# Kernel tuning notes

Measured on AMD Instinct MI355X. Metric: run time of the kernel, lower is better.

## Reference

```python
import jax, jax.numpy as jnp
import numpy as np

N = 50000      # nodes
E = 800000     # edges
CIN = 128
CH = 128
COUT = 64
EPS = 1e-5     # BatchNorm eps


def setup_inputs() -> dict:
    key = jax.random.key(0)
    ks = jax.random.split(key, 16)
    s = 0.1  # weight scale for numerical stability
    return {
        "x": jax.random.normal(ks[0], (N, CIN), jnp.float32),
        "edge_index": jax.random.randint(ks[1], (2, E), 0, N, jnp.int32),
        "edge_weights": jax.random.uniform(ks[2], (E,), jnp.float32),
        "w1": jax.random.normal(ks[3], (CIN, CH), jnp.float32) * s,
        "b1": jnp.zeros((CH,), jnp.float32),
        "bn1_g": jnp.ones((CH,), jnp.float32),
        "bn1_b": jnp.zeros((CH,), jnp.float32),
        "bn1_m": jax.random.normal(ks[4], (CH,), jnp.float32) * 0.1,
        "bn1_v": jax.random.uniform(ks[5], (CH,), jnp.float32) + 0.5,
        "conv_ws": jax.random.normal(ks[6], (2, CH, CH), jnp.float32) * s,
        "conv_bs": jnp.zeros((2, CH), jnp.float32),
        "bns_g": jnp.ones((2, CH), jnp.float32),
        "bns_b": jnp.zeros((2, CH), jnp.float32),
        "bns_m": jax.random.normal(ks[7], (2, CH), jnp.float32) * 0.1,
        "bns_v": jax.random.uniform(ks[8], (2, CH), jnp.float32) + 0.5,
        "lin1_w": jax.random.normal(ks[9], (CH, CH), jnp.float32) * s,
        "lin1_b": jnp.zeros((CH,), jnp.float32),
        "lin2_w": jax.random.normal(ks[10], (CH, COUT), jnp.float32) * s,
        "lin2_b": jnp.zeros((COUT,), jnp.float32),
    }


def _bn(h, g, b, m, v):
    # BatchNorm1d in eval mode: running statistics
    return (h - m) * jax.lax.rsqrt(v + EPS) * g + b


def _gcn(h, w, b, src, dst, norm, n):
    # GCNConv: out[dst] += norm_e * (h @ W)[src]  (self loops already in src/dst)
    h = h @ w
    msg = h[src] * norm[:, None]                 # [E+N, CH]
    return jax.ops.segment_sum(msg, dst, num_segments=n) + b


def reference(x, edge_index, edge_weights, w1, b1, bn1_g, bn1_b, bn1_m, bn1_v,
              conv_ws, conv_bs, bns_g, bns_b, bns_m, bns_v,
              lin1_w, lin1_b, lin2_w, lin2_b):
    n = x.shape[0]
    loop = jnp.arange(n, dtype=edge_index.dtype)
    src = jnp.concatenate([edge_index[0], loop])
    dst = jnp.concatenate([edge_index[1], loop])
    ew = jnp.concatenate([edge_weights, jnp.ones((n,), edge_weights.dtype)])
    # symmetric degree normalization (PyG gcn_norm)
    deg = jax.ops.segment_sum(ew, dst, num_segments=n)
    dis = jnp.where(deg > 0, jax.lax.rsqrt(deg), 0.0)
    norm = dis[src] * ew * dis[dst]

    lrelu = jax.nn.leaky_relu  # slope 0.01, matches F.leaky_relu default
    h = lrelu(_bn(_gcn(x, w1, b1, src, dst, norm, n), bn1_g, bn1_b, bn1_m, bn1_v))
    for i in range(conv_ws.shape[0]):
        h = lrelu(_bn(_gcn(h, conv_ws[i], conv_bs[i], src, dst, norm, n),
                      bns_g[i], bns_b[i], bns_m[i], bns_v[i]) + h)
    h = lrelu(h @ lin1_w + lin1_b)
    # dropout is identity in eval mode
    return h @ lin2_w + lin2_b
```

## Files before the change

### kernel.cpp

```cpp
#include <hip/hip_runtime.h>
#include <hip/hip_bf16.h>


constexpr int   NN    = 50000;
constexpr int   EE    = 800000;
constexpr int   CH    = 128;
constexpr int   SLOTS = 64;
constexpr int   NBUK  = 782;
constexpr int   RCAP  = 2048;
constexpr int   EPB   = 2048;
constexpr float EPS   = 1e-5f;

typedef __attribute__((ext_vector_type(8))) short bf16x8;
typedef __attribute__((ext_vector_type(4))) float f32x4;
typedef unsigned long long u64;
typedef unsigned short u16;

__device__ inline u16 f2bf_rne(float f) {
  unsigned u = __float_as_uint(f);
  unsigned r = u + 0x7fffu + ((u >> 16) & 1u);
  return (u16)(r >> 16);
}
__device__ inline float bf2f(unsigned h16) {
  return __uint_as_float(h16 << 16);
}


__global__ __launch_bounds__(256) void bin_kernel(const int* __restrict__ ei,
                                                  const float* __restrict__ ew,
                                                  unsigned* __restrict__ gcur,
                                                  u64* __restrict__ bins) {
  __shared__ unsigned cnt[NBUK];
  __shared__ unsigned base[NBUK];
  const int tid = threadIdx.x;
  for (int b = tid; b < NBUK; b += 256) cnt[b] = 0;
  __syncthreads();
  const int e0 = blockIdx.x * EPB;
  unsigned pk[8]; u16 bkt[8]; u16 rnk[8]; unsigned char dl[8];
  #pragma unroll
  for (int i = 0; i < 8; i++) {
    int e = e0 + i * 256 + tid;
    if (e < EE) {
      int s = ei[e], d = ei[EE + e];
      float w = ew[e];
      bkt[i] = (u16)(d >> 6);
      dl[i]  = (unsigned char)(d & 63);
      pk[i]  = ((unsigned)f2bf_rne(w) << 16) | (unsigned)s;
      rnk[i] = (u16)atomicAdd(&cnt[bkt[i]], 1u);
    } else bkt[i] = 0xffffu;
  }
  __syncthreads();
  for (int b = tid; b < NBUK; b += 256) {
    unsigned c = cnt[b];
    base[b] = c ? atomicAdd(&gcur[b * 16], c) : 0u;
  }
  __syncthreads();
  #pragma unroll
  for (int i = 0; i < 8; i++) {
    if (bkt[i] == 0xffffu) continue;
    unsigned pos = base[bkt[i]] + rnk[i];
    if (pos < RCAP)
      bins[(size_t)bkt[i] * RCAP + pos] = ((u64)dl[i] << 32) | pk[i];
  }
}


__global__ __launch_bounds__(256) void scatter_kernel(const unsigned* __restrict__ gcur,
                                                      const u64* __restrict__ bins,
                                                      unsigned* __restrict__ ell,
                                                      float* __restrict__ dis) {
  __shared__ unsigned rank[64];
  __shared__ float    wsum[64];
  const int b   = blockIdx.x;
  const int tid = threadIdx.x;
  if (tid < 64) { rank[tid] = 1u; wsum[tid] = 0.f; }
  __syncthreads();
  unsigned cnt = gcur[b * 16];
  if (cnt > RCAP) cnt = RCAP;
  const u64* src = bins + (size_t)b * RCAP;
  for (unsigned i = tid; i < cnt; i += 256) {
    u64 v = src[i];
    unsigned pk = (unsigned)v;
    unsigned dl = (unsigned)(v >> 32);
    unsigned r = atomicAdd(&rank[dl], 1u);
    if (r < SLOTS)
      ell[((size_t)(b * 64 + dl)) * SLOTS + r] = pk;
    atomicAdd(&wsum[dl], bf2f(pk >> 16));
  }
  __syncthreads();
  if (tid < 64) {
    int node = b * 64 + tid;
    if (node < NN) {
      unsigned c = rank[tid];
      if (c > SLOTS) c = SLOTS;
      ell[(size_t)node * SLOTS] = c;
      dis[node] = rsqrtf(1.0f + wsum[tid]);
    }
  }
}

constexpr int NB_WZ = (73728 + 384 + 255) / 256;

__global__ void wswz_kernel(
    const float* __restrict__ w1, const float* __restrict__ bn1_g, const float* __restrict__ bn1_v,
    const float* __restrict__ conv_ws, const float* __restrict__ bns_g, const float* __restrict__ bns_v,
    const float* __restrict__ lin1_w, const float* __restrict__ lin2_w,
    const float* __restrict__ b1, const float* __restrict__ bn1_b, const float* __restrict__ bn1_m,
    const float* __restrict__ conv_bs, const float* __restrict__ bns_b, const float* __restrict__ bns_m,
    u16* __restrict__ w1h, u16* __restrict__ w1l,
    u16* __restrict__ c0h, u16* __restrict__ c0l,
    u16* __restrict__ c1h, u16* __restrict__ c1l,
    u16* __restrict__ l1h, u16* __restrict__ l1l,
    u16* __restrict__ l2h, u16* __restrict__ l2l,
    float* __restrict__ beff)
{
  int idx = blockIdx.x * 256 + threadIdx.x;
  if (idx >= 73728) {
    int r = idx - 73728;
    if (r >= 384) return;
    int l = r >> 7, c = r & 127;
    float bc, gg, bb, mm, vv;
    if (l == 0) { bc = b1[c]; gg = bn1_g[c]; bb = bn1_b[c]; mm = bn1_m[c]; vv = bn1_v[c]; }
    else {
      int o = (l - 1) * 128 + c;
      bc = conv_bs[o]; gg = bns_g[o]; bb = bns_b[o]; mm = bns_m[o]; vv = bns_v[o];
    }
    beff[r] = (bc - mm) * gg * rsqrtf(vv + EPS) + bb;
    return;
  }
  const float* W; const float* g = nullptr; const float* v = nullptr;
  u16 *hi, *lo; int CO = 128; int local;
  if      (idx < 16384) { W = w1;              g = bn1_g;     v = bn1_v;     hi = w1h; lo = w1l; local = idx; }
  else if (idx < 32768) { W = conv_ws;         g = bns_g;     v = bns_v;     hi = c0h; lo = c0l; local = idx - 16384; }
  else if (idx < 49152) { W = conv_ws + 16384; g = bns_g+128; v = bns_v+128; hi = c1h; lo = c1l; local = idx - 32768; }
  else if (idx < 65536) { W = lin1_w;                                        hi = l1h; lo = l1l; local = idx - 49152; }
  else                  { W = lin2_w;                                        hi = l2h; lo = l2l; local = idx - 65536; CO = 64; }
  int k = local / CO, n = local % CO;
  float w = W[local];
  if (g) w *= g[n] * rsqrtf(v[n] + EPS);
  int NCT = CO / 16;
  int kchunk = k >> 5, kin = k & 31, quad = kin >> 3, j = kin & 7;
  int ct = n >> 4, l = (quad << 4) | (n & 15);
  size_t pos = ((size_t)(kchunk * NCT + ct) * 64 + l) * 8 + j;
  u16 h = f2bf_rne(w);
  hi[pos] = h;
  lo[pos] = f2bf_rne(w - bf2f(h));
}

__global__ __launch_bounds__(256) void gemm1_kernel(
    const float* __restrict__ Ain,
    const u16* __restrict__ Whi, const u16* __restrict__ Wlo,
    const float* __restrict__ dis, u16* __restrict__ Cout)
{
  __shared__ float lds[64][CH + 4];
  const int tid  = threadIdx.x;
  const int wave = tid >> 6;
  const int lane = tid & 63;
  const int quad = lane >> 4;
  const int mrow = lane & 15;
  const int row0 = blockIdx.x * 64;

  int arow = row0 + wave * 16 + mrow;
  if (arow >= NN) arow = NN - 1;

  bf16x8 ahi[4], alo[4];
  const float* Ar = Ain + (size_t)arow * CH;
  #pragma unroll
  for (int c = 0; c < 4; c++) {
    int off = c * 32 + quad * 8;
    float4 f0 = *(const float4*)(Ar + off);
    float4 f1 = *(const float4*)(Ar + off + 4);
    float f[8] = {f0.x, f0.y, f0.z, f0.w, f1.x, f1.y, f1.z, f1.w};
    #pragma unroll
    for (int j = 0; j < 8; j++) {
      u16 h = f2bf_rne(f[j]);
      ahi[c][j] = (short)h;
      alo[c][j] = (short)f2bf_rne(f[j] - bf2f(h));
    }
  }

  f32x4 acc[8];
  #pragma unroll
  for (int t = 0; t < 8; t++) acc[t] = (f32x4){0.f, 0.f, 0.f, 0.f};
  #pragma unroll
  for (int c = 0; c < 4; c++) {
    #pragma unroll
    for (int t = 0; t < 8; t++) {
      size_t base = ((size_t)(c * 8 + t) * 64 + lane) * 8;
      bf16x8 bh = *(const bf16x8*)(Whi + base);
      bf16x8 bl = *(const bf16x8*)(Wlo + base);
      acc[t] = __builtin_amdgcn_mfma_f32_16x16x32_bf16(ahi[c], bh, acc[t], 0, 0, 0);
      acc[t] = __builtin_amdgcn_mfma_f32_16x16x32_bf16(alo[c], bh, acc[t], 0, 0, 0);
      acc[t] = __builtin_amdgcn_mfma_f32_16x16x32_bf16(ahi[c], bl, acc[t], 0, 0, 0);
    }
  }

  #pragma unroll
  for (int t = 0; t < 8; t++)
    #pragma unroll
    for (int r = 0; r < 4; r++)
      lds[wave * 16 + quad * 4 + r][t * 16 + mrow] = acc[t][r];
  __syncthreads();

  #pragma unroll
  for (int i = tid; i < 64 * CH / 4; i += 256) {
    int row = (i * 4) / CH;
    int col = (i * 4) % CH;
    int grow = row0 + row;
    if (grow >= NN) continue;
    float rs = dis[grow];
    const float* lp = &lds[row][col];
    u16* cp = (u16*)Cout + (size_t)grow * CH + col;
    unsigned p0 = ((unsigned)f2bf_rne(lp[1] * rs) << 16) | f2bf_rne(lp[0] * rs);
    unsigned p1 = ((unsigned)f2bf_rne(lp[3] * rs) << 16) | f2bf_rne(lp[2] * rs);
    *(uint2*)cp = make_uint2(p0, p1);
  }
}

template<bool RES, bool WH>
__device__ __forceinline__ void gather4_grp(
    const u16* __restrict__ hwin, const unsigned* __restrict__ ell,
    const float* __restrict__ dis, const float* __restrict__ beff,
    const u16* __restrict__ res, u16* __restrict__ hout,
    unsigned* __restrict__ hsbase,
    int nbase, int lane, int sub, int grp)
{
  const int node = nbase + grp;
  const size_t ebase = (size_t)node * SLOTS + sub;
  unsigned w0 = ell[ebase];
  unsigned w1 = ell[ebase + 16];
  unsigned w2 = ell[ebase + 32];
  unsigned w3 = ell[ebase + 48];

  int cme = __shfl((int)w0, grp << 4); if (cme > SLOTS) cme = SLOTS;
  int c0 = __shfl((int)w0, 0),  c1 = __shfl((int)w0, 16);
  int c2 = __shfl((int)w0, 32), c3 = __shfl((int)w0, 48);
  int cmax = max(max(c0, c1), max(c2, c3)); if (cmax > SLOTS) cmax = SLOTS;

  float a[8] = {0.f, 0.f, 0.f, 0.f, 0.f, 0.f, 0.f, 0.f};
  const u16* hrow = hwin + sub * 8;

  for (int j = 0; j < cmax; j += 8) {
    uint4 hQ[8]; float wQ[8];
    #pragma unroll
    for (int u = 0; u < 8; u++) {
      int jj = j + u;
      int k = jj >> 4;
      unsigned wsel = k == 0 ? w0 : (k == 1 ? w1 : (k == 2 ? w2 : w3));
      unsigned e = (unsigned)__shfl((int)wsel, (grp << 4) | (jj & 15));
      float wv = (jj == 0) ? 1.0f : bf2f(e >> 16);
      unsigned s = (jj == 0) ? (unsigned)node : (e & 0xffffu);
      if (jj >= cme) { wv = 0.f; s = (unsigned)node; }
      wQ[u] = wv;
      hQ[u] = *(const uint4*)(hrow + (size_t)s * CH);
    }
    #pragma unroll
    for (int u = 0; u < 8; u++) {
      float w = wQ[u];
      a[0] = fmaf(w, bf2f(hQ[u].x & 0xffffu), a[0]); a[1] = fmaf(w, bf2f(hQ[u].x >> 16), a[1]);
      a[2] = fmaf(w, bf2f(hQ[u].y & 0xffffu), a[2]); a[3] = fmaf(w, bf2f(hQ[u].y >> 16), a[3]);
      a[4] = fmaf(w, bf2f(hQ[u].z & 0xffffu), a[4]); a[5] = fmaf(w, bf2f(hQ[u].z >> 16), a[5]);
      a[6] = fmaf(w, bf2f(hQ[u].w & 0xffffu), a[6]); a[7] = fmaf(w, bf2f(hQ[u].w >> 16), a[7]);
    }
  }

  float disd = dis[node];
  int c = sub * 8;
  float4 be0 = *(const float4*)(beff + c);
  float4 be1 = *(const float4*)(beff + c + 4);
  float y[8];
  y[0] = a[0] * disd + be0.x; y[1] = a[1] * disd + be0.y;
  y[2] = a[2] * disd + be0.z; y[3] = a[3] * disd + be0.w;
  y[4] = a[4] * disd + be1.x; y[5] = a[5] * disd + be1.y;
  y[6] = a[6] * disd + be1.z; y[7] = a[7] * disd + be1.w;
  if constexpr (RES) {
    uint4 rr = *(const uint4*)(res + (size_t)node * CH + c);
    y[0] += bf2f(rr.x & 0xffffu); y[1] += bf2f(rr.x >> 16);
    y[2] += bf2f(rr.y & 0xffffu); y[3] += bf2f(rr.y >> 16);
    y[4] += bf2f(rr.z & 0xffffu); y[5] += bf2f(rr.z >> 16);
    y[6] += bf2f(rr.w & 0xffffu); y[7] += bf2f(rr.w >> 16);
  }
  #pragma unroll
  for (int k = 0; k < 8; k++) y[k] = y[k] > 0.f ? y[k] : 0.01f * y[k];
  uint4 o;
  o.x = ((unsigned)f2bf_rne(y[1]) << 16) | f2bf_rne(y[0]);
  o.y = ((unsigned)f2bf_rne(y[3]) << 16) | f2bf_rne(y[2]);
  o.z = ((unsigned)f2bf_rne(y[5]) << 16) | f2bf_rne(y[4]);
  o.w = ((unsigned)f2bf_rne(y[7]) << 16) | f2bf_rne(y[6]);
  if constexpr (WH)
    *(uint4*)(hout + (size_t)node * CH + c) = o;
  *(uint4*)&hsbase[grp * 68 + sub * 4] = o;
}

template<bool RES>
__global__ __launch_bounds__(256, 6) void fuse_kernel(
    const u16* __restrict__ hwin,
    const unsigned* __restrict__ ell, const float* __restrict__ dis,
    const float* __restrict__ beff, const u16* __restrict__ res,
    const u16* __restrict__ Whi, const u16* __restrict__ Wlo,
    u16* __restrict__ hout, u16* __restrict__ hwout)
{
  __shared__ unsigned hs[16][68];
  const int tid  = threadIdx.x;
  const int wave = tid >> 6;
  const int lane = tid & 63;
  const int sub  = lane & 15;
  const int grp  = lane >> 4;
  const int row0 = blockIdx.x * 16;

  gather4_grp<RES, true>(hwin, ell, dis, beff, res, hout,
                         &hs[wave * 4][0], row0 + wave * 4, lane, sub, grp);
  __syncthreads();

  bf16x8 af[4];
  #pragma unroll
  for (int c = 0; c < 4; c++)
    af[c] = *(const bf16x8*)&hs[sub][c * 16 + grp * 4];

  f32x4 acc[2];
  #pragma unroll
  for (int t = 0; t < 2; t++) acc[t] = (f32x4){0.f, 0.f, 0.f, 0.f};
  #pragma unroll
  for (int c = 0; c < 4; c++) {
    #pragma unroll
    for (int t = 0; t < 2; t++) {
      size_t base = ((size_t)(c * 8 + wave * 2 + t) * 64 + lane) * 8;
      bf16x8 bh = *(const bf16x8*)(Whi + base);
      bf16x8 bl = *(const bf16x8*)(Wlo + base);
      acc[t] = __builtin_amdgcn_mfma_f32_16x16x32_bf16(af[c], bh, acc[t], 0, 0, 0);
      acc[t] = __builtin_amdgcn_mfma_f32_16x16x32_bf16(af[c], bl, acc[t], 0, 0, 0);
    }
  }

  #pragma unroll
  for (int r = 0; r < 4; r++) {
    int grow = row0 + grp * 4 + r;
    if (grow >= NN) continue;
    float rs = dis[grow];
    #pragma unroll
    for (int t = 0; t < 2; t++)
      hwout[(size_t)grow * CH + wave * 32 + t * 16 + sub] = f2bf_rne(acc[t][r] * rs);
  }
}

__global__ __launch_bounds__(256, 6) void fuse_last_kernel(
    const u16* __restrict__ hwin,
    const unsigned* __restrict__ ell, const float* __restrict__ dis,
    const float* __restrict__ beff, const u16* __restrict__ res,
    const u16* __restrict__ l1h, const u16* __restrict__ l1l,
    const float* __restrict__ b1,
    const u16* __restrict__ l2h, const u16* __restrict__ l2l,
    const float* __restrict__ b2, float* __restrict__ out)
{
  __shared__ unsigned hs[16][68];
  __shared__ float    fs[16][132];
  const int tid  = threadIdx.x;
  const int wave = tid >> 6;
  const int lane = tid & 63;
  const int sub  = lane & 15;
  const int grp  = lane >> 4;
  const int row0 = blockIdx.x * 16;

  gather4_grp<true, false>(hwin, ell, dis, beff, res, nullptr,
                           &hs[wave * 4][0], row0 + wave * 4, lane, sub, grp);
  __syncthreads();

  bf16x8 af[4];
  #pragma unroll
  for (int c = 0; c < 4; c++)
    af[c] = *(const bf16x8*)&hs[sub][c * 16 + grp * 4];

  f32x4 acc[2];
  #pragma unroll
  for (int t = 0; t < 2; t++) acc[t] = (f32x4){0.f, 0.f, 0.f, 0.f};
  #pragma unroll
  for (int c = 0; c < 4; c++) {
    #pragma unroll
    for (int t = 0; t < 2; t++) {
      size_t base = ((size_t)(c * 8 + wave * 2 + t) * 64 + lane) * 8;
      bf16x8 bh = *(const bf16x8*)(l1h + base);
      bf16x8 bl = *(const bf16x8*)(l1l + base);
      acc[t] = __builtin_amdgcn_mfma_f32_16x16x32_bf16(af[c], bh, acc[t], 0, 0, 0);
      acc[t] = __builtin_amdgcn_mfma_f32_16x16x32_bf16(af[c], bl, acc[t], 0, 0, 0);
    }
  }
  #pragma unroll
  for (int t = 0; t < 2; t++) {
    int col = wave * 32 + t * 16 + sub;
    float bb = b1[col];
    #pragma unroll
    for (int r = 0; r < 4; r++) {
      float x = acc[t][r] + bb;
      x = x > 0.f ? x : 0.01f * x;
      fs[grp * 4 + r][col] = x;
    }
  }
  __syncthreads();

  f32x4 acc2 = (f32x4){0.f, 0.f, 0.f, 0.f};
  #pragma unroll
  for (int c = 0; c < 4; c++) {
    bf16x8 ahi, alo;
    const float* lp = &fs[sub][c * 32 + grp * 8];
    float4 f0 = *(const float4*)lp;
    float4 f1 = *(const float4*)(lp + 4);
    float f[8] = {f0.x, f0.y, f0.z, f0.w, f1.x, f1.y, f1.z, f1.w};
    #pragma unroll
    for (int j = 0; j < 8; j++) {
      u16 h = f2bf_rne(f[j]);
      ahi[j] = (short)h;
      alo[j] = (short)f2bf_rne(f[j] - bf2f(h));
    }
    size_t base = ((size_t)(c * 4 + wave) * 64 + lane) * 8;
    bf16x8 bh = *(const bf16x8*)(l2h + base);
    bf16x8 bl = *(const bf16x8*)(l2l + base);
    acc2 = __builtin_amdgcn_mfma_f32_16x16x32_bf16(ahi, bh, acc2, 0, 0, 0);
    acc2 = __builtin_amdgcn_mfma_f32_16x16x32_bf16(alo, bh, acc2, 0, 0, 0);
    acc2 = __builtin_amdgcn_mfma_f32_16x16x32_bf16(ahi, bl, acc2, 0, 0, 0);
  }
  {
    float bb = b2[wave * 16 + sub];
    #pragma unroll
    for (int r = 0; r < 4; r++) {
      int grow = row0 + grp * 4 + r;
      if (grow < NN)
        out[(size_t)grow * 64 + wave * 16 + sub] = acc2[r] + bb;
    }
  }
}


extern "C" void kernel_launch(void* const* d_in, const int* in_sizes, int n_in,
                              void* d_out, int out_size, void* d_ws, size_t ws_size,
                              hipStream_t stream) {
  const float* x       = (const float*)d_in[0];
  const int*   ei      = (const int*)  d_in[1];
  const float* ew      = (const float*)d_in[2];
  const float* w1      = (const float*)d_in[3];
  const float* b1      = (const float*)d_in[4];
  const float* bn1_g   = (const float*)d_in[5];
  const float* bn1_b   = (const float*)d_in[6];
  const float* bn1_m   = (const float*)d_in[7];
  const float* bn1_v   = (const float*)d_in[8];
  const float* conv_ws = (const float*)d_in[9];
  const float* conv_bs = (const float*)d_in[10];
  const float* bns_g   = (const float*)d_in[11];
  const float* bns_b   = (const float*)d_in[12];
  const float* bns_m   = (const float*)d_in[13];
  const float* bns_v   = (const float*)d_in[14];
  const float* lin1_w  = (const float*)d_in[15];
  const float* lin1_b  = (const float*)d_in[16];
  const float* lin2_w  = (const float*)d_in[17];
  const float* lin2_b  = (const float*)d_in[18];
  float* out = (float*)d_out;

  size_t off = 0;
  auto alloc = [&](size_t elems) -> void* {
    void* p = (char*)d_ws + off * 4;
    off += (elems + 3) & ~(size_t)3;
    return p;
  };
  unsigned* gcur = (unsigned*)alloc(NBUK * 16);
  u64*      bins = (u64*)     alloc((size_t)NBUK * RCAP * 2);
  unsigned* ell  = (unsigned*)alloc((size_t)NN * SLOTS);
  float*    dis  = (float*)   alloc(NN);
  float*    beff = (float*)   alloc(3 * CH);
  u16*      hwa  = (u16*)     alloc((size_t)NN * CH / 2);
  u16*      hwb  = (u16*)     alloc((size_t)NN * CH / 2);
  u16*      h1   = (u16*)     alloc((size_t)NN * CH / 2);
  u16*      h2   = (u16*)     alloc((size_t)NN * CH / 2);
  u16* w1h = (u16*)alloc(CH * CH / 2); u16* w1l = (u16*)alloc(CH * CH / 2);
  u16* c0h = (u16*)alloc(CH * CH / 2); u16* c0l = (u16*)alloc(CH * CH / 2);
  u16* c1h = (u16*)alloc(CH * CH / 2); u16* c1l = (u16*)alloc(CH * CH / 2);
  u16* l1h = (u16*)alloc(CH * CH / 2); u16* l1l = (u16*)alloc(CH * CH / 2);
  u16* l2h = (u16*)alloc(CH * 64 / 2); u16* l2l = (u16*)alloc(CH * 64 / 2);

  const int nb_bin  = (EE + EPB - 1) / EPB;
  const int nb_gemm = (NN + 63) / 64;
  const int nb_fuse = (NN + 15) / 16;
  dim3 B(256);

  hipMemsetAsync(gcur, 0, NBUK * 16 * sizeof(unsigned), stream);
  bin_kernel    <<<nb_bin, B, 0, stream>>>(ei, ew, gcur, bins);
  scatter_kernel<<<NBUK,   B, 0, stream>>>(gcur, bins, ell, dis);

  wswz_kernel<<<NB_WZ, B, 0, stream>>>(w1, bn1_g, bn1_v, conv_ws, bns_g, bns_v,
      lin1_w, lin2_w, b1, bn1_b, bn1_m, conv_bs, bns_b, bns_m,
      w1h, w1l, c0h, c0l, c1h, c1l, l1h, l1l, l2h, l2l, beff);

  gemm1_kernel<<<nb_gemm, B, 0, stream>>>(x, w1h, w1l, dis, hwa);

  fuse_kernel<false><<<nb_fuse, B, 0, stream>>>(hwa, ell, dis, beff, nullptr,
      c0h, c0l, h1, hwb);

  fuse_kernel<true><<<nb_fuse, B, 0, stream>>>(hwb, ell, dis, beff + CH, h1,
      c1h, c1l, h2, hwa);

  fuse_last_kernel<<<nb_fuse, B, 0, stream>>>(hwa, ell, dis, beff + 2 * CH, h2,
      l1h, l1l, lin1_b, l2h, l2l, lin2_b, out);
}
```

Before: 333.7 us.

## Fuse binning with weight swizzle and scatter with first GEMM; stage fuse stores

Merges the edge-binning kernel and the weight-swizzle kernel into one launch by giving each a separate block range. It also fuses the ELL scatter and degree computation with the first GEMM, since both use 64-node blocks, so dis is taken from shared memory instead of global. In fuse_kernel, outputs are staged through LDS and written as coalesced 16-byte stores, which adds extra barriers. Together this removes two launches and reduces uncoalesced 2-byte global writes.

```diff
diff --git a/kernel.cpp b/kernel.cpp
--- a/kernel.cpp
+++ b/kernel.cpp
@@ -9,6 +9,8 @@
 constexpr int   NBUK  = 782;
 constexpr int   RCAP  = 2048;
 constexpr int   EPB   = 2048;
+constexpr int   NB_BIN = (EE + EPB - 1) / EPB;
+constexpr int   NB_WZ  = (73728 + 384 + 255) / 256;
 constexpr float EPS   = 1e-5f;
 
 typedef __attribute__((ext_vector_type(8))) short bf16x8;
@@ -26,82 +28,9 @@
 }
 
 
-__global__ __launch_bounds__(256) void bin_kernel(const int* __restrict__ ei,
-                                                  const float* __restrict__ ew,
-                                                  unsigned* __restrict__ gcur,
-                                                  u64* __restrict__ bins) {
-  __shared__ unsigned cnt[NBUK];
-  __shared__ unsigned base[NBUK];
-  const int tid = threadIdx.x;
-  for (int b = tid; b < NBUK; b += 256) cnt[b] = 0;
-  __syncthreads();
-  const int e0 = blockIdx.x * EPB;
-  unsigned pk[8]; u16 bkt[8]; u16 rnk[8]; unsigned char dl[8];
-  #pragma unroll
-  for (int i = 0; i < 8; i++) {
-    int e = e0 + i * 256 + tid;
-    if (e < EE) {
-      int s = ei[e], d = ei[EE + e];
-      float w = ew[e];
-      bkt[i] = (u16)(d >> 6);
-      dl[i]  = (unsigned char)(d & 63);
-      pk[i]  = ((unsigned)f2bf_rne(w) << 16) | (unsigned)s;
-      rnk[i] = (u16)atomicAdd(&cnt[bkt[i]], 1u);
-    } else bkt[i] = 0xffffu;
-  }
-  __syncthreads();
-  for (int b = tid; b < NBUK; b += 256) {
-    unsigned c = cnt[b];
-    base[b] = c ? atomicAdd(&gcur[b * 16], c) : 0u;
-  }
-  __syncthreads();
-  #pragma unroll
-  for (int i = 0; i < 8; i++) {
-    if (bkt[i] == 0xffffu) continue;
-    unsigned pos = base[bkt[i]] + rnk[i];
-    if (pos < RCAP)
-      bins[(size_t)bkt[i] * RCAP + pos] = ((u64)dl[i] << 32) | pk[i];
-  }
-}
-
-
-__global__ __launch_bounds__(256) void scatter_kernel(const unsigned* __restrict__ gcur,
-                                                      const u64* __restrict__ bins,
-                                                      unsigned* __restrict__ ell,
-                                                      float* __restrict__ dis) {
-  __shared__ unsigned rank[64];
-  __shared__ float    wsum[64];
-  const int b   = blockIdx.x;
-  const int tid = threadIdx.x;
-  if (tid < 64) { rank[tid] = 1u; wsum[tid] = 0.f; }
-  __syncthreads();
-  unsigned cnt = gcur[b * 16];
-  if (cnt > RCAP) cnt = RCAP;
-  const u64* src = bins + (size_t)b * RCAP;
-  for (unsigned i = tid; i < cnt; i += 256) {
-    u64 v = src[i];
-    unsigned pk = (unsigned)v;
-    unsigned dl = (unsigned)(v >> 32);
-    unsigned r = atomicAdd(&rank[dl], 1u);
-    if (r < SLOTS)
-      ell[((size_t)(b * 64 + dl)) * SLOTS + r] = pk;
-    atomicAdd(&wsum[dl], bf2f(pk >> 16));
-  }
-  __syncthreads();
-  if (tid < 64) {
-    int node = b * 64 + tid;
-    if (node < NN) {
-      unsigned c = rank[tid];
-      if (c > SLOTS) c = SLOTS;
-      ell[(size_t)node * SLOTS] = c;
-      dis[node] = rsqrtf(1.0f + wsum[tid]);
-    }
-  }
-}
-
-constexpr int NB_WZ = (73728 + 384 + 255) / 256;
-
-__global__ void wswz_kernel(
+__global__ __launch_bounds__(256) void binw_kernel(
+    const int* __restrict__ ei, const float* __restrict__ ew,
+    unsigned* __restrict__ gcur, u64* __restrict__ bins,
     const float* __restrict__ w1, const float* __restrict__ bn1_g, const float* __restrict__ bn1_v,
     const float* __restrict__ conv_ws, const float* __restrict__ bns_g, const float* __restrict__ bns_v,
     const float* __restrict__ lin1_w, const float* __restrict__ lin2_w,
@@ -114,51 +43,122 @@
     u16* __restrict__ l2h, u16* __restrict__ l2l,
     float* __restrict__ beff)
 {
-  int idx = blockIdx.x * 256 + threadIdx.x;
-  if (idx >= 73728) {
-    int r = idx - 73728;
-    if (r >= 384) return;
-    int l = r >> 7, c = r & 127;
-    float bc, gg, bb, mm, vv;
-    if (l == 0) { bc = b1[c]; gg = bn1_g[c]; bb = bn1_b[c]; mm = bn1_m[c]; vv = bn1_v[c]; }
-    else {
-      int o = (l - 1) * 128 + c;
-      bc = conv_bs[o]; gg = bns_g[o]; bb = bns_b[o]; mm = bns_m[o]; vv = bns_v[o];
-    }
-    beff[r] = (bc - mm) * gg * rsqrtf(vv + EPS) + bb;
+  const int tid = threadIdx.x;
+  if (blockIdx.x >= NB_BIN) {
+    int idx = (blockIdx.x - NB_BIN) * 256 + tid;
+    if (idx >= 73728) {
+      int r = idx - 73728;
+      if (r >= 384) return;
+      int l = r >> 7, c = r & 127;
+      float bc, gg, bb, mm, vv;
+      if (l == 0) { bc = b1[c]; gg = bn1_g[c]; bb = bn1_b[c]; mm = bn1_m[c]; vv = bn1_v[c]; }
+      else {
+        int o = (l - 1) * 128 + c;
+        bc = conv_bs[o]; gg = bns_g[o]; bb = bns_b[o]; mm = bns_m[o]; vv = bns_v[o];
+      }
+      beff[r] = (bc - mm) * gg * rsqrtf(vv + EPS) + bb;
+      return;
+    }
+    const float* W; const float* g = nullptr; const float* v = nullptr;
+    u16 *hi, *lo; int CO = 128; int local;
+    if      (idx < 16384) { W = w1;              g = bn1_g;     v = bn1_v;     hi = w1h; lo = w1l; local = idx; }
+    else if (idx < 32768) { W = conv_ws;         g = bns_g;     v = bns_v;     hi = c0h; lo = c0l; local = idx - 16384; }
+    else if (idx < 49152) { W = conv_ws + 16384; g = bns_g+128; v = bns_v+128; hi = c1h; lo = c1l; local = idx - 32768; }
+    else if (idx < 65536) { W = lin1_w;                                        hi = l1h; lo = l1l; local = idx - 49152; }
+    else                  { W = lin2_w;                                        hi = l2h; lo = l2l; local = idx - 65536; CO = 64; }
+    int k = local / CO, n = local % CO;
+    float w = W[local];
+    if (g) w *= g[n] * rsqrtf(v[n] + EPS);
+    int NCT = CO / 16;
+    int kchunk = k >> 5, kin = k & 31, quad = kin >> 3, j = kin & 7;
+    int ct = n >> 4, l = (quad << 4) | (n & 15);
+    size_t pos = ((size_t)(kchunk * NCT + ct) * 64 + l) * 8 + j;
+    u16 h = f2bf_rne(w);
+    hi[pos] = h;
+    lo[pos] = f2bf_rne(w - bf2f(h));
     return;
   }
-  const float* W; const float* g = nullptr; const float* v = nullptr;
-  u16 *hi, *lo; int CO = 128; int local;
-  if      (idx < 16384) { W = w1;              g = bn1_g;     v = bn1_v;     hi = w1h; lo = w1l; local = idx; }
-  else if (idx < 32768) { W = conv_ws;         g = bns_g;     v = bns_v;     hi = c0h; lo = c0l; local = idx - 16384; }
-  else if (idx < 49152) { W = conv_ws + 16384; g = bns_g+128; v = bns_v+128; hi = c1h; lo = c1l; local = idx - 32768; }
-  else if (idx < 65536) { W = lin1_w;                                        hi = l1h; lo = l1l; local = idx - 49152; }
-  else                  { W = lin2_w;                                        hi = l2h; lo = l2l; local = idx - 65536; CO = 64; }
-  int k = local / CO, n = local % CO;
-  float w = W[local];
-  if (g) w *= g[n] * rsqrtf(v[n] + EPS);
-  int NCT = CO / 16;
-  int kchunk = k >> 5, kin = k & 31, quad = kin >> 3, j = kin & 7;
-  int ct = n >> 4, l = (quad << 4) | (n & 15);
-  size_t pos = ((size_t)(kchunk * NCT + ct) * 64 + l) * 8 + j;
-  u16 h = f2bf_rne(w);
-  hi[pos] = h;
-  lo[pos] = f2bf_rne(w - bf2f(h));
-}
-
-__global__ __launch_bounds__(256) void gemm1_kernel(
+  __shared__ unsigned cnt[NBUK];
+  __shared__ unsigned base[NBUK];
+  for (int b = tid; b < NBUK; b += 256) cnt[b] = 0;
+  __syncthreads();
+  const int e0 = blockIdx.x * EPB;
+  unsigned pk[8]; u16 bkt[8]; u16 rnk[8]; unsigned char dl[8];
+  #pragma unroll
+  for (int i = 0; i < 8; i++) {
+    int e = e0 + i * 256 + tid;
+    if (e < EE) {
+      int s = ei[e], d = ei[EE + e];
+      float w = ew[e];
+      bkt[i] = (u16)(d >> 6);
+      dl[i]  = (unsigned char)(d & 63);
+      pk[i]  = ((unsigned)f2bf_rne(w) << 16) | (unsigned)s;
+      rnk[i] = (u16)atomicAdd(&cnt[bkt[i]], 1u);
+    } else bkt[i] = 0xffffu;
+  }
+  __syncthreads();
+  for (int b = tid; b < NBUK; b += 256) {
+    unsigned c = cnt[b];
+    base[b] = c ? atomicAdd(&gcur[b * 16], c) : 0u;
+  }
+  __syncthreads();
+  #pragma unroll
+  for (int i = 0; i < 8; i++) {
+    if (bkt[i] == 0xffffu) continue;
+    unsigned pos = base[bkt[i]] + rnk[i];
+    if (pos < RCAP)
+      bins[(size_t)bkt[i] * RCAP + pos] = ((u64)dl[i] << 32) | pk[i];
+  }
+}
+
+
+__global__ __launch_bounds__(256) void scatgemm_kernel(
+    const unsigned* __restrict__ gcur, const u64* __restrict__ bins,
+    unsigned* __restrict__ ell, float* __restrict__ dis,
     const float* __restrict__ Ain,
     const u16* __restrict__ Whi, const u16* __restrict__ Wlo,
-    const float* __restrict__ dis, u16* __restrict__ Cout)
+    u16* __restrict__ Cout)
 {
-  __shared__ float lds[64][CH + 4];
-  const int tid  = threadIdx.x;
+  __shared__ unsigned rank[64];
+  __shared__ float    wsum[64];
+  __shared__ float    disl[64];
+  __shared__ float    lds[64][CH + 4];
+  const int b   = blockIdx.x;
+  const int tid = threadIdx.x;
+
+  if (tid < 64) { rank[tid] = 1u; wsum[tid] = 0.f; }
+  __syncthreads();
+  unsigned cnt = gcur[b * 16];
+  if (cnt > RCAP) cnt = RCAP;
+  const u64* src = bins + (size_t)b * RCAP;
+  for (unsigned i = tid; i < cnt; i += 256) {
+    u64 v = src[i];
+    unsigned pk = (unsigned)v;
+    unsigned dl = (unsigned)(v >> 32);
+    unsigned r = atomicAdd(&rank[dl], 1u);
+    if (r < SLOTS)
+      ell[((size_t)(b * 64 + dl)) * SLOTS + r] = pk;
+    atomicAdd(&wsum[dl], bf2f(pk >> 16));
+  }
+  __syncthreads();
+  if (tid < 64) {
+    int node = b * 64 + tid;
+    float d = rsqrtf(1.0f + wsum[tid]);
+    disl[tid] = d;
+    if (node < NN) {
+      unsigned c = rank[tid];
+      if (c > SLOTS) c = SLOTS;
+      ell[(size_t)node * SLOTS] = c;
+      dis[node] = d;
+    }
+  }
+  __syncthreads();
+
   const int wave = tid >> 6;
   const int lane = tid & 63;
   const int quad = lane >> 4;
   const int mrow = lane & 15;
-  const int row0 = blockIdx.x * 64;
+  const int row0 = b * 64;
 
   int arow = row0 + wave * 16 + mrow;
   if (arow >= NN) arow = NN - 1;
@@ -208,7 +208,7 @@
     int col = (i * 4) % CH;
     int grow = row0 + row;
     if (grow >= NN) continue;
-    float rs = dis[grow];
+    float rs = disl[row];
     const float* lp = &lds[row][col];
     u16* cp = (u16*)Cout + (size_t)grow * CH + col;
     unsigned p0 = ((unsigned)f2bf_rne(lp[1] * rs) << 16) | f2bf_rne(lp[0] * rs);
@@ -316,6 +316,7 @@
   #pragma unroll
   for (int c = 0; c < 4; c++)
     af[c] = *(const bf16x8*)&hs[sub][c * 16 + grp * 4];
+  __syncthreads();
 
   f32x4 acc[2];
   #pragma unroll
@@ -332,14 +333,21 @@
     }
   }
 
+  u16* hs16 = (u16*)&hs[0][0];
   #pragma unroll
   for (int r = 0; r < 4; r++) {
-    int grow = row0 + grp * 4 + r;
-    if (grow >= NN) continue;
-    float rs = dis[grow];
+    int row = grp * 4 + r;
+    float rs = dis[row0 + row];
     #pragma unroll
     for (int t = 0; t < 2; t++)
-      hwout[(size_t)grow * CH + wave * 32 + t * 16 + sub] = f2bf_rne(acc[t][r] * rs);
+      hs16[row * 136 + wave * 32 + t * 16 + sub] = f2bf_rne(acc[t][r] * rs);
+  }
+  __syncthreads();
+  {
+    int row   = tid >> 4;
+    int chunk = tid & 15;
+    uint4 o = *(const uint4*)(hs16 + row * 136 + chunk * 8);
+    *(uint4*)(hwout + (size_t)(row0 + row) * CH + chunk * 8) = o;
   }
 }
 
@@ -475,20 +483,17 @@
   u16* l1h = (u16*)alloc(CH * CH / 2); u16* l1l = (u16*)alloc(CH * CH / 2);
   u16* l2h = (u16*)alloc(CH * 64 / 2); u16* l2l = (u16*)alloc(CH * 64 / 2);
 
-  const int nb_bin  = (EE + EPB - 1) / EPB;
-  const int nb_gemm = (NN + 63) / 64;
   const int nb_fuse = (NN + 15) / 16;
   dim3 B(256);
 
   hipMemsetAsync(gcur, 0, NBUK * 16 * sizeof(unsigned), stream);
-  bin_kernel    <<<nb_bin, B, 0, stream>>>(ei, ew, gcur, bins);
-  scatter_kernel<<<NBUK,   B, 0, stream>>>(gcur, bins, ell, dis);
-
-  wswz_kernel<<<NB_WZ, B, 0, stream>>>(w1, bn1_g, bn1_v, conv_ws, bns_g, bns_v,
-      lin1_w, lin2_w, b1, bn1_b, bn1_m, conv_bs, bns_b, bns_m,
+
+  binw_kernel<<<NB_BIN + NB_WZ, B, 0, stream>>>(ei, ew, gcur, bins,
+      w1, bn1_g, bn1_v, conv_ws, bns_g, bns_v, lin1_w, lin2_w,
+      b1, bn1_b, bn1_m, conv_bs, bns_b, bns_m,
       w1h, w1l, c0h, c0l, c1h, c1l, l1h, l1l, l2h, l2l, beff);
 
-  gemm1_kernel<<<nb_gemm, B, 0, stream>>>(x, w1h, w1l, dis, hwa);
+  scatgemm_kernel<<<NBUK, B, 0, stream>>>(gcur, bins, ell, dis, x, w1h, w1l, hwa);
 
   fuse_kernel<false><<<nb_fuse, B, 0, stream>>>(hwa, ell, dis, beff, nullptr,
       c0h, c0l, h1, hwb);
```

Result: faster. 320.2 us (-4.1%).
